# Kernel optimization log

Hardware: AMD Instinct MI355X
Metric: run time of the kernel (lower is better)

## Reference

```python
import jax, jax.numpy as jnp
import numpy as np

N = 50000
E = 800000
NUM_GRAPHS = 64

def gat_layer(x, W, att_src, att_dst, bias, src, dst, heads, out_ch, concat):
    n = x.shape[0]
    h = (x @ W).reshape(n, heads, out_ch)                      # [N,H,C]
    a_s = jnp.sum(h * att_src, axis=-1)                        # [N,H]
    a_d = jnp.sum(h * att_dst, axis=-1)                        # [N,H]
    e = jax.nn.leaky_relu(a_s[src] + a_d[dst], 0.2)            # [E,H]
    m = jax.ops.segment_max(e, dst, num_segments=n)            # segment softmax (self-loops guarantee non-empty)
    e = jnp.exp(e - m[dst])
    s = jax.ops.segment_sum(e, dst, num_segments=n)
    alpha = e / s[dst]                                         # [E,H]
    out = jax.ops.segment_sum(alpha[:, :, None] * h[src], dst, num_segments=n)  # [N,H,C]
    out = out.reshape(n, heads * out_ch) if concat else out.mean(axis=1)
    return out + bias

def setup_inputs() -> dict:
    key = jax.random.key(0)
    ks = jax.random.split(key, 20)
    inp = {}
    inp['x'] = jax.random.normal(ks[0], (N, 256), dtype=jnp.float32)
    inp['edge_index'] = jax.random.randint(ks[1], (2, E), 0, N, dtype=jnp.int64)
    inp['batch'] = jnp.sort(jax.random.randint(ks[2], (N,), 0, NUM_GRAPHS, dtype=jnp.int64))
    s = 0.05
    inp['W1'] = jax.random.normal(ks[3], (256, 256), dtype=jnp.float32) * s
    inp['att_src1'] = jax.random.normal(ks[4], (8, 32), dtype=jnp.float32) * s
    inp['att_dst1'] = jax.random.normal(ks[5], (8, 32), dtype=jnp.float32) * s
    inp['b1'] = jax.random.normal(ks[6], (256,), dtype=jnp.float32) * s
    inp['W2'] = jax.random.normal(ks[7], (256, 256), dtype=jnp.float32) * s
    inp['att_src2'] = jax.random.normal(ks[8], (8, 32), dtype=jnp.float32) * s
    inp['att_dst2'] = jax.random.normal(ks[9], (8, 32), dtype=jnp.float32) * s
    inp['b2'] = jax.random.normal(ks[10], (256,), dtype=jnp.float32) * s
    inp['W3'] = jax.random.normal(ks[11], (256, 32), dtype=jnp.float32) * s
    inp['att_src3'] = jax.random.normal(ks[12], (1, 32), dtype=jnp.float32) * s
    inp['att_dst3'] = jax.random.normal(ks[13], (1, 32), dtype=jnp.float32) * s
    inp['b3'] = jax.random.normal(ks[14], (32,), dtype=jnp.float32) * s
    inp['linW'] = jax.random.normal(ks[15], (32, 1), dtype=jnp.float32) * s
    inp['linb'] = jax.random.normal(ks[16], (1,), dtype=jnp.float32) * s
    return inp

def reference(x, edge_index, batch, W1, att_src1, att_dst1, b1, W2, att_src2, att_dst2, b2,
              W3, att_src3, att_dst3, b3, linW, linb):
    # add self loops (PyG add_self_loops=True)
    loop = jnp.arange(N, dtype=edge_index.dtype)
    src = jnp.concatenate([edge_index[0], loop])
    dst = jnp.concatenate([edge_index[1], loop])
    # eval mode: dropout is identity
    h = gat_layer(x, W1, att_src1, att_dst1, b1, src, dst, 8, 32, True)
    h = jax.nn.elu(h)
    h = gat_layer(h, W2, att_src2, att_dst2, b2, src, dst, 8, 32, True)
    h = jax.nn.elu(h)
    h = gat_layer(h, W3, att_src3, att_dst3, b3, src, dst, 1, 32, False)
    # global mean pool over all nodes (topic_mask defaults to all True)
    sums = jax.ops.segment_sum(h, batch, num_segments=NUM_GRAPHS)
    cnts = jax.ops.segment_sum(jnp.ones((N,), h.dtype), batch, num_segments=NUM_GRAPHS)
    pooled = sums / jnp.maximum(cnts, 1.0)[:, None]
    out = pooled @ linW + linb                                  # [G,1]
    return out.squeeze(-1)                                      # num_classes==2
```

## Files before the change

kernel.cpp:

```cpp
#include <hip/hip_runtime.h>
#include <hip/hip_fp8.h>
#include <math.h>


typedef __attribute__((ext_vector_type(8))) __bf16 bf16x8;
typedef __attribute__((ext_vector_type(4))) __bf16 bf16x4;
typedef __attribute__((ext_vector_type(4))) float f32x4;
typedef __attribute__((ext_vector_type(2))) float f32x2;

#define SCAN_CH 4

__device__ inline unsigned char f32_to_fp8(float f) {
  __hip_fp8_e4m3 v(f);
  return (unsigned char)v.__x;
}
__device__ inline float fp8_to_f32(unsigned char u) {
  __hip_fp8_e4m3 v;
  v.__x = (__hip_fp8_storage_t)u;
  return (float)v;
}

__device__ inline void fma_fp8x4(f32x4& acc, float w, unsigned int packed) {
#if defined(__has_builtin) && __has_builtin(__builtin_amdgcn_cvt_pk_f32_fp8)
  f32x2 lo = __builtin_amdgcn_cvt_pk_f32_fp8((int)packed, false);
  f32x2 hi = __builtin_amdgcn_cvt_pk_f32_fp8((int)packed, true);
  acc[0] += w * lo[0];
  acc[1] += w * lo[1];
  acc[2] += w * hi[0];
  acc[3] += w * hi[1];
#else
  acc[0] += w * fp8_to_f32((unsigned char)(packed & 0xff));
  acc[1] += w * fp8_to_f32((unsigned char)((packed >> 8) & 0xff));
  acc[2] += w * fp8_to_f32((unsigned char)((packed >> 16) & 0xff));
  acc[3] += w * fp8_to_f32((unsigned char)(packed >> 24));
#endif
}

__global__ __launch_bounds__(256) void k_init_deg(int* deg, int N) {
  int n = blockIdx.x * 256 + threadIdx.x;
  if (n < N) deg[n] = 1;
}

__global__ __launch_bounds__(256) void k_count_deg(const int* __restrict__ ei,
                                                   int E, int* deg) {
  int e = blockIdx.x * 256 + threadIdx.x;
  if (e < E) atomicAdd(&deg[ei[E + e]], 1);
}

__global__ __launch_bounds__(256) void k_scan_partial(const int* __restrict__ deg,
                                                      int* __restrict__ blockSums,
                                                      int N) {
  __shared__ int sh[256];
  int t = threadIdx.x, b = blockIdx.x;
  int base = (b * 256 + t) * SCAN_CH;
  int s = 0;
#pragma unroll
  for (int j = 0; j < SCAN_CH; j++) {
    int idx = base + j;
    if (idx < N) s += deg[idx];
  }
  sh[t] = s;
  __syncthreads();
  for (int off = 128; off > 0; off >>= 1) {
    if (t < off) sh[t] += sh[t + off];
    __syncthreads();
  }
  if (t == 0) blockSums[b] = sh[0];
}

__global__ __launch_bounds__(256) void k_scan_blocksums(
    const int* __restrict__ blockSums, int* __restrict__ blockOffs,
    int* __restrict__ rowptr, int nb, int N) {
  __shared__ int sh[256];
  int t = threadIdx.x;
  int v = (t < nb) ? blockSums[t] : 0;
  sh[t] = v;
  __syncthreads();
  for (int off = 1; off < 256; off <<= 1) {
    int u = (t >= off) ? sh[t - off] : 0;
    __syncthreads();
    sh[t] += u;
    __syncthreads();
  }
  if (t < nb) blockOffs[t] = sh[t] - v;
  if (t == nb - 1) rowptr[N] = sh[t];
}

__global__ __launch_bounds__(256) void k_scan_final(const int* __restrict__ deg,
                                                    const int* __restrict__ blockOffs,
                                                    int* __restrict__ rowptr,
                                                    int* __restrict__ cursor, int N) {
  __shared__ int sh[256];
  int t = threadIdx.x, b = blockIdx.x;
  int base = (b * 256 + t) * SCAN_CH;
  int vals[SCAN_CH];
  int s = 0;
#pragma unroll
  for (int j = 0; j < SCAN_CH; j++) {
    int idx = base + j;
    vals[j] = (idx < N) ? deg[idx] : 0;
    s += vals[j];
  }
  sh[t] = s;
  __syncthreads();
  for (int off = 1; off < 256; off <<= 1) {
    int u = (t >= off) ? sh[t - off] : 0;
    __syncthreads();
    sh[t] += u;
    __syncthreads();
  }
  int run = blockOffs[b] + sh[t] - s;
#pragma unroll
  for (int j = 0; j < SCAN_CH; j++) {
    int idx = base + j;
    if (idx < N) {
      rowptr[idx] = run;
      cursor[idx] = run;
      run += vals[j];
    }
  }
}

__global__ __launch_bounds__(256) void k_scatter2(const int* __restrict__ ei,
                                                  int E, int N, int* cursor,
                                                  int2* __restrict__ col2,
                                                  int* __restrict__ col_s,
                                                  int chunkSz) {
  int stripe = blockIdx.x & 7;
  int chunk = blockIdx.x >> 3;
  int lo = (int)(((long long)N * stripe) >> 3);
  int hi = (int)(((long long)N * (stripe + 1)) >> 3);
  int base = chunk * chunkSz;
  int end = base + chunkSz;
  int total = E + N;
  if (end > total) end = total;
  for (int i = base + threadIdx.x; i < end; i += 256) {
    int d = (i < E) ? ei[E + i] : (i - E);
    if (d < lo || d >= hi) continue;
    int s = (i < E) ? ei[i] : d;
    int pos = atomicAdd(&cursor[d], 1);
    col2[pos] = make_int2(s, d);
    col_s[pos] = s;
  }
}

__global__ __launch_bounds__(256) void k_cast(const float* __restrict__ in,
                                              __bf16* __restrict__ oh, int n4) {
  int i = blockIdx.x * 256 + threadIdx.x;
  if (i >= n4) return;
  float4 v = ((const float4*)in)[i];
  bf16x4 h;
  h[0] = (__bf16)v.x;
  h[1] = (__bf16)v.y;
  h[2] = (__bf16)v.z;
  h[3] = (__bf16)v.w;
  ((bf16x4*)oh)[i] = h;
}

__global__ __launch_bounds__(256) void k_wprep(const float* __restrict__ W,
                                               __bf16* __restrict__ WTh,
                                               int K, int Nc) {
  int i = blockIdx.x * 256 + threadIdx.x;
  if (i >= K * Nc) return;
  int n = i / K, k = i - n * K;
  WTh[i] = (__bf16)W[k * Nc + n];
}

__global__ __launch_bounds__(256) void k_gemm_sA(
    const __bf16* __restrict__ Ah, const __bf16* __restrict__ BTh,
    __bf16* __restrict__ Ch, unsigned char* __restrict__ Cf8, int M, int K) {
  constexpr int NcFull = 256;
  __shared__ __bf16 sA[64 * 256];
  int tid = threadIdx.x;
  int lane = tid & 63, wave = tid >> 6;
  int quad = lane >> 4, l16 = lane & 15;
  int m0 = blockIdx.x * 64;
  int col0 = wave * 64;
  int srow = tid >> 2;
  int mtw = srow >> 4, l16w = srow & 15;
  int arow = min(m0 + srow, M - 1);
  const __bf16* ag = Ah + (size_t)arow * K;
#pragma unroll
  for (int r = 0; r < 8; r++) {
    int c = (tid & 3) + r * 4;
    int s = c >> 2, q = c & 3;
    int slot = (((s * 4 + mtw) * 4 + q) * 16 + l16w) * 8;
    *(bf16x8*)(sA + slot) = *(const bf16x8*)(ag + c * 8);
  }
  __syncthreads();
  const __bf16* brh = BTh + (size_t)(col0 + l16) * K + quad * 8;
  f32x4 acc[4][4];
#pragma unroll
  for (int mt = 0; mt < 4; mt++)
#pragma unroll
    for (int t = 0; t < 4; t++) acc[mt][t] = (f32x4){0.f, 0.f, 0.f, 0.f};
  for (int s = 0; s < 8; s++) {
    bf16x8 b_h[4];
#pragma unroll
    for (int t = 0; t < 4; t++)
      b_h[t] = *(const bf16x8*)(brh + (size_t)t * 16 * K + s * 32);
    bf16x8 a_h[4];
#pragma unroll
    for (int mt = 0; mt < 4; mt++)
      a_h[mt] = *(const bf16x8*)(sA + (((s * 4 + mt) * 4 + quad) * 16 + l16) * 8);
#pragma unroll
    for (int t = 0; t < 4; t++) {
#pragma unroll
      for (int mt = 0; mt < 4; mt++) {
        acc[mt][t] = __builtin_amdgcn_mfma_f32_16x16x32_bf16(a_h[mt], b_h[t], acc[mt][t], 0, 0, 0);
      }
    }
  }
#pragma unroll
  for (int mt = 0; mt < 4; mt++) {
#pragma unroll
    for (int t = 0; t < 4; t++) {
#pragma unroll
      for (int r = 0; r < 4; r++) {
        int m = m0 + mt * 16 + quad * 4 + r;
        if (m < M) {
          size_t o = (size_t)m * NcFull + col0 + t * 16 + l16;
          Ch[o] = (__bf16)acc[mt][t][r];
          Cf8[o] = f32_to_fp8(acc[mt][t][r]);
        }
      }
    }
  }
}

template <int NT, int MT>
__global__ __launch_bounds__(256) void k_gemm_split(
    const __bf16* __restrict__ Ah, const __bf16* __restrict__ BTh,
    __bf16* __restrict__ Ch, int M, int K, int NcFull) {
  int lane = threadIdx.x & 63;
  int wave = threadIdx.x >> 6;
  int quad = lane >> 4;
  int l16 = lane & 15;
  int m0 = blockIdx.y * (64 * MT) + wave * (16 * MT);
  int col0 = blockIdx.x * (NT * 16);
  const __bf16* arh[MT];
#pragma unroll
  for (int mt = 0; mt < MT; mt++) {
    int am = min(m0 + mt * 16 + l16, M - 1);
    arh[mt] = Ah + (size_t)am * K + quad * 8;
  }
  const __bf16* brh = BTh + (size_t)(col0 + l16) * K + quad * 8;
  f32x4 acc[MT][NT];
#pragma unroll
  for (int mt = 0; mt < MT; mt++)
#pragma unroll
    for (int t = 0; t < NT; t++) acc[mt][t] = (f32x4){0.f, 0.f, 0.f, 0.f};
  for (int k0 = 0; k0 < K; k0 += 32) {
    bf16x8 a_h[MT], b_h[NT];
#pragma unroll
    for (int mt = 0; mt < MT; mt++) {
      a_h[mt] = *(const bf16x8*)(arh[mt] + k0);
    }
#pragma unroll
    for (int t = 0; t < NT; t++)
      b_h[t] = *(const bf16x8*)(brh + (size_t)t * 16 * K + k0);
#pragma unroll
    for (int t = 0; t < NT; t++) {
#pragma unroll
      for (int mt = 0; mt < MT; mt++) {
        acc[mt][t] = __builtin_amdgcn_mfma_f32_16x16x32_bf16(a_h[mt], b_h[t], acc[mt][t], 0, 0, 0);
      }
    }
  }
#pragma unroll
  for (int mt = 0; mt < MT; mt++) {
#pragma unroll
    for (int t = 0; t < NT; t++) {
#pragma unroll
      for (int r = 0; r < 4; r++) {
        int m = m0 + mt * 16 + quad * 4 + r;
        if (m < M)
          Ch[(size_t)m * NcFull + col0 + t * 16 + l16] = (__bf16)acc[mt][t][r];
      }
    }
  }
}

__global__ __launch_bounds__(256) void k_att(const __bf16* __restrict__ Hh,
                                             const float* __restrict__ attS,
                                             const float* __restrict__ attD,
                                             float* __restrict__ aS,
                                             float* __restrict__ aD, int NH, int H) {
  int idx = blockIdx.x * 256 + threadIdx.x;
  if (idx >= NH) return;
  int h = idx % H;
  const bf16x8* hv = (const bf16x8*)(Hh + (size_t)idx * 32);
  const float* sv = attS + h * 32;
  const float* dv = attD + h * 32;
  float ss = 0.f, dd = 0.f;
#pragma unroll
  for (int k = 0; k < 4; k++) {
    bf16x8 a = hv[k];
#pragma unroll
    for (int j = 0; j < 8; j++) {
      float v = (float)a[j];
      ss += v * sv[k * 8 + j];
      dd += v * dv[k * 8 + j];
    }
  }
  aS[idx] = ss;
  aD[idx] = dd;
}

__global__ __launch_bounds__(256) void k_edge_alpha8(
    const float* __restrict__ aS, const float* __restrict__ aD,
    const int2* __restrict__ col2,
    __bf16* __restrict__ ealpha, int M) {
  int e = blockIdx.x * 256 + threadIdx.x;
  if (e >= M) return;
  int2 sd = col2[e];
  const float* ap = aS + (size_t)sd.x * 8;
  const float* dp = aD + (size_t)sd.y * 8;
  bf16x8 ev;
#pragma unroll
  for (int h = 0; h < 8; h++) {
    float x = ap[h] + dp[h];
    x = (x > 0.f) ? x : 0.2f * x;
    ev[h] = (__bf16)__expf(x);
  }
  *(bf16x8*)(ealpha + (size_t)e * 8) = ev;
}

__global__ __launch_bounds__(256) void k_edge_alpha1(
    const float* __restrict__ aS, const float* __restrict__ aD,
    const int2* __restrict__ col2,
    __bf16* __restrict__ ealpha, int M) {
  int e = blockIdx.x * 256 + threadIdx.x;
  if (e >= M) return;
  int2 sd = col2[e];
  float x = aS[sd.x] + aD[sd.y];
  x = (x > 0.f) ? x : 0.2f * x;
  ealpha[e] = (__bf16)__expf(x);
}

__global__ __launch_bounds__(256) void k_gat_agg8(
    const unsigned char* __restrict__ Hf8, const int* __restrict__ rowptr,
    const int* __restrict__ col_s, const __bf16* __restrict__ ealpha,
    const float* __restrict__ bias, __bf16* __restrict__ outh, int N) {
  int wid = (blockIdx.x * blockDim.x + threadIdx.x) >> 6;
  int lane = threadIdx.x & 63;
  if (wid >= N) return;
  int n = wid;
  int row0 = rowptr[n];
  int deg = rowptr[n + 1] - row0;
  int head = lane >> 3;

  f32x4 acc = (f32x4){0.f, 0.f, 0.f, 0.f};
  float den = 0.f;
  const __bf16* ea = ealpha;
  int i = 0;
  for (; i + 3 < deg; i += 4) {
    int sl = row0 + i;
    int s0 = col_s[sl + 0];
    int s1 = col_s[sl + 1];
    int s2 = col_s[sl + 2];
    int s3 = col_s[sl + 3];
    float w0 = (float)ea[(size_t)(sl + 0) * 8 + head];
    float w1 = (float)ea[(size_t)(sl + 1) * 8 + head];
    float w2 = (float)ea[(size_t)(sl + 2) * 8 + head];
    float w3 = (float)ea[(size_t)(sl + 3) * 8 + head];
    unsigned int p0 = *(const unsigned int*)(Hf8 + (size_t)s0 * 256 + lane * 4);
    unsigned int p1 = *(const unsigned int*)(Hf8 + (size_t)s1 * 256 + lane * 4);
    unsigned int p2 = *(const unsigned int*)(Hf8 + (size_t)s2 * 256 + lane * 4);
    unsigned int p3 = *(const unsigned int*)(Hf8 + (size_t)s3 * 256 + lane * 4);
    den += w0 + w1 + w2 + w3;
    fma_fp8x4(acc, w0, p0);
    fma_fp8x4(acc, w1, p1);
    fma_fp8x4(acc, w2, p2);
    fma_fp8x4(acc, w3, p3);
  }
  for (; i < deg; i++) {
    int sl = row0 + i;
    int s0 = col_s[sl];
    float w0 = (float)ea[(size_t)sl * 8 + head];
    unsigned int p0 = *(const unsigned int*)(Hf8 + (size_t)s0 * 256 + lane * 4);
    den += w0;
    fma_fp8x4(acc, w0, p0);
  }
  float rsv = 1.f / den;
  float4 bv = *(const float4*)(bias + lane * 4);
  bf16x4 hb;
#pragma unroll
  for (int j = 0; j < 4; j++) {
    float v = acc[j] * rsv + ((const float*)&bv)[j];
    v = (v > 0.f) ? v : (__expf(v) - 1.f);
    hb[j] = (__bf16)v;
  }
  *(bf16x4*)(outh + (size_t)n * 256 + lane * 4) = hb;
}

__global__ __launch_bounds__(256) void k_gat_agg1(
    const __bf16* __restrict__ Hh, const int* __restrict__ rowptr,
    const int* __restrict__ col_s, const __bf16* __restrict__ ealpha,
    const float* __restrict__ bias, float* __restrict__ out, int N) {
  int wid = (blockIdx.x * blockDim.x + threadIdx.x) >> 6;
  int lane = threadIdx.x & 63;
  if (wid >= N) return;
  int n = wid;
  int row0 = rowptr[n];
  int deg = rowptr[n + 1] - row0;
  int eo = lane >> 3;
  int cl = lane & 7;
  f32x4 acc = (f32x4){0.f, 0.f, 0.f, 0.f};
  float den = 0.f;
  for (int i = eo; i < deg; i += 8) {
    int slot = row0 + i;
    int src = col_s[slot];
    float w = (float)ealpha[slot];
    den += w;
    bf16x4 hv = *(const bf16x4*)(Hh + (size_t)src * 32 + cl * 4);
#pragma unroll
    for (int j = 0; j < 4; j++) acc[j] += w * (float)hv[j];
  }
#pragma unroll
  for (int off = 8; off < 64; off <<= 1) {
#pragma unroll
    for (int j = 0; j < 4; j++) acc[j] += __shfl_xor(acc[j], off, 64);
    den += __shfl_xor(den, off, 64);
  }
  if (eo == 0) {
    float rsv = 1.f / den;
#pragma unroll
    for (int j = 0; j < 4; j++)
      out[(size_t)n * 32 + cl * 4 + j] = acc[j] * rsv + bias[cl * 4 + j];
  }
}

__global__ __launch_bounds__(256) void k_pool_final(
    const float* __restrict__ h, const int* __restrict__ batch,
    const float* __restrict__ linW, const float* __restrict__ linb,
    float* __restrict__ out, int N) {
  __shared__ float sh[256];
  int g = blockIdx.x;
  int tid = threadIdx.x;
  int grp = tid >> 5, c = tid & 31;
  int lo = 0, hi = N;
  while (lo < hi) { int mid = (lo + hi) >> 1; if (batch[mid] < g) lo = mid + 1; else hi = mid; }
  int start = lo;
  hi = N;
  while (lo < hi) { int mid = (lo + hi) >> 1; if (batch[mid] < g + 1) lo = mid + 1; else hi = mid; }
  int end = lo;
  float acc = 0.f;
  for (int n = start + grp; n < end; n += 8) acc += h[(size_t)n * 32 + c];
  sh[tid] = acc;
  __syncthreads();
  if (tid < 32) {
    float s = 0.f;
#pragma unroll
    for (int j = 0; j < 8; j++) s += sh[j * 32 + tid];
    float v = s * linW[tid];
#pragma unroll
    for (int off = 16; off > 0; off >>= 1) v += __shfl_xor(v, off, 64);
    if (tid == 0) {
      float cnt = (float)(end - start);
      out[g] = v / fmaxf(cnt, 1.f) + linb[0];
    }
  }
}

extern "C" void kernel_launch(void* const* d_in, const int* in_sizes, int n_in,
                              void* d_out, int out_size, void* d_ws, size_t ws_size,
                              hipStream_t stream) {
  const float* x = (const float*)d_in[0];
  const int* ei = (const int*)d_in[1];
  const int* batch = (const int*)d_in[2];
  const float* W1 = (const float*)d_in[3];
  const float* as1 = (const float*)d_in[4];
  const float* ad1 = (const float*)d_in[5];
  const float* b1 = (const float*)d_in[6];
  const float* W2 = (const float*)d_in[7];
  const float* as2 = (const float*)d_in[8];
  const float* ad2 = (const float*)d_in[9];
  const float* b2 = (const float*)d_in[10];
  const float* W3 = (const float*)d_in[11];
  const float* as3 = (const float*)d_in[12];
  const float* ad3 = (const float*)d_in[13];
  const float* b3 = (const float*)d_in[14];
  const float* linW = (const float*)d_in[15];
  const float* linb = (const float*)d_in[16];

  const int N = in_sizes[0] / 256;
  const int E = in_sizes[1] / 2;
  const int NUM_GRAPHS = 64;
  float* out = (float*)d_out;

  char* ws = (char*)d_ws;
  size_t off = 0;
  auto alloc = [&](size_t bytes) -> void* {
    void* p = ws + off;
    off += (bytes + 255) & ~(size_t)255;
    return p;
  };
  __bf16* Hh = (__bf16*)alloc((size_t)N * 256 * 2);
  unsigned char* Hf8 = (unsigned char*)alloc((size_t)N * 256);
  __bf16* Ah = (__bf16*)alloc((size_t)N * 256 * 2);
  __bf16* ealpha = (__bf16*)alloc((size_t)(E + N) * 8 * 2);
  float* aS = (float*)alloc((size_t)N * 8 * 4);
  float* aD = (float*)alloc((size_t)N * 8 * 4);
  int* deg = (int*)alloc((size_t)N * 4);
  int* rowptr = (int*)alloc((size_t)(N + 1) * 4);
  int* cursor = (int*)alloc((size_t)(N + 1) * 4);
  int2* col2 = (int2*)alloc((size_t)(E + N) * 8);
  int* col_s = (int*)alloc((size_t)(E + N) * 4);
  int* blockSums = (int*)alloc(256 * 4);
  int* blockOffs = (int*)alloc(256 * 4);
  __bf16* WT1h = (__bf16*)alloc(256 * 256 * 2);
  __bf16* WT2h = (__bf16*)alloc(256 * 256 * 2);
  __bf16* WT3h = (__bf16*)alloc(32 * 256 * 2);
  float* h3agg = (float*)Ah;

  k_cast<<<(N * 64 + 255) / 256, 256, 0, stream>>>(x, Ah, N * 64);
  k_wprep<<<(256 * 256 + 255) / 256, 256, 0, stream>>>(W1, WT1h, 256, 256);
  k_wprep<<<(256 * 256 + 255) / 256, 256, 0, stream>>>(W2, WT2h, 256, 256);
  k_wprep<<<(256 * 32 + 255) / 256, 256, 0, stream>>>(W3, WT3h, 256, 32);
  k_init_deg<<<(N + 255) / 256, 256, 0, stream>>>(deg, N);
  k_count_deg<<<(E + 255) / 256, 256, 0, stream>>>(ei, E, deg);
  const int nb = (N + 256 * SCAN_CH - 1) / (256 * SCAN_CH);
  k_scan_partial<<<nb, 256, 0, stream>>>(deg, blockSums, N);
  k_scan_blocksums<<<1, 256, 0, stream>>>(blockSums, blockOffs, rowptr, nb, N);
  k_scan_final<<<nb, 256, 0, stream>>>(deg, blockOffs, rowptr, cursor, N);
  {
    const int totalItems = E + N;
    const int nch = 256;
    const int chunkSz = (totalItems + nch - 1) / nch;
    k_scatter2<<<8 * nch, 256, 0, stream>>>(ei, E, N, cursor, col2, col_s, chunkSz);
  }

  const int aggBlocks = (N + 3) / 4;
  const int gemmBlocks = (N + 63) / 64;
  const int M = E + N;
  const int edgeBlocks = (M + 255) / 256;
  dim3 g3(1, (N + 63) / 64);

  k_gemm_sA<<<gemmBlocks, 256, 0, stream>>>(Ah, WT1h, Hh, Hf8, N, 256);
  k_att<<<(N * 8 + 255) / 256, 256, 0, stream>>>(Hh, as1, ad1, aS, aD, N * 8, 8);
  k_edge_alpha8<<<edgeBlocks, 256, 0, stream>>>(aS, aD, col2, ealpha, M);
  k_gat_agg8<<<aggBlocks, 256, 0, stream>>>(Hf8, rowptr, col_s, ealpha, b1,
                                            Ah, N);
  k_gemm_sA<<<gemmBlocks, 256, 0, stream>>>(Ah, WT2h, Hh, Hf8, N, 256);
  k_att<<<(N * 8 + 255) / 256, 256, 0, stream>>>(Hh, as2, ad2, aS, aD, N * 8, 8);
  k_edge_alpha8<<<edgeBlocks, 256, 0, stream>>>(aS, aD, col2, ealpha, M);
  k_gat_agg8<<<aggBlocks, 256, 0, stream>>>(Hf8, rowptr, col_s, ealpha, b2,
                                            Ah, N);
  k_gemm_split<2, 1><<<g3, 256, 0, stream>>>(Ah, WT3h, Hh, N, 256, 32);
  k_att<<<(N + 255) / 256, 256, 0, stream>>>(Hh, as3, ad3, aS, aD, N, 1);
  k_edge_alpha1<<<edgeBlocks, 256, 0, stream>>>(aS, aD, col2, ealpha, M);
  k_gat_agg1<<<aggBlocks, 256, 0, stream>>>(Hh, rowptr, col_s, ealpha, b3,
                                            h3agg, N);
  k_pool_final<<<NUM_GRAPHS, 256, 0, stream>>>(h3agg, batch, linW, linb, out, N);
}
```

Baseline: 483.0 us.

## Fuse edge attention weights into aggregation and drop col_s array

Removes the separate edge-alpha kernels and computes each edge's leaky-relu and exp inside the aggregation kernels from aS and aD. This avoids writing and re-reading the per-edge bf16 alpha buffer and saves three launches. The 8-head aggregation is restructured so each wave handles 4 edges at a time, with 16 lanes each loading 16 fp8 bytes and a shuffle reduction at the end. The col_s array is dropped and sources are read from col2. The trade-off is exp work repeated per lane, strided int2 reads, and extra shuffle reductions.

```diff
diff --git a/kernel.cpp b/kernel.cpp
--- a/kernel.cpp
+++ b/kernel.cpp
@@ -124,7 +124,6 @@
 __global__ __launch_bounds__(256) void k_scatter2(const int* __restrict__ ei,
                                                   int E, int N, int* cursor,
                                                   int2* __restrict__ col2,
-                                                  int* __restrict__ col_s,
                                                   int chunkSz) {
   int stripe = blockIdx.x & 7;
   int chunk = blockIdx.x >> 3;
@@ -140,7 +139,6 @@
     int s = (i < E) ? ei[i] : d;
     int pos = atomicAdd(&cursor[d], 1);
     col2[pos] = make_int2(s, d);
-    col_s[pos] = s;
   }
 }
 
@@ -307,97 +305,98 @@
   aD[idx] = dd;
 }
 
-__global__ __launch_bounds__(256) void k_edge_alpha8(
-    const float* __restrict__ aS, const float* __restrict__ aD,
-    const int2* __restrict__ col2,
-    __bf16* __restrict__ ealpha, int M) {
-  int e = blockIdx.x * 256 + threadIdx.x;
-  if (e >= M) return;
-  int2 sd = col2[e];
-  const float* ap = aS + (size_t)sd.x * 8;
-  const float* dp = aD + (size_t)sd.y * 8;
-  bf16x8 ev;
-#pragma unroll
-  for (int h = 0; h < 8; h++) {
-    float x = ap[h] + dp[h];
-    x = (x > 0.f) ? x : 0.2f * x;
-    ev[h] = (__bf16)__expf(x);
-  }
-  *(bf16x8*)(ealpha + (size_t)e * 8) = ev;
-}
-
-__global__ __launch_bounds__(256) void k_edge_alpha1(
-    const float* __restrict__ aS, const float* __restrict__ aD,
-    const int2* __restrict__ col2,
-    __bf16* __restrict__ ealpha, int M) {
-  int e = blockIdx.x * 256 + threadIdx.x;
-  if (e >= M) return;
-  int2 sd = col2[e];
-  float x = aS[sd.x] + aD[sd.y];
-  x = (x > 0.f) ? x : 0.2f * x;
-  ealpha[e] = (__bf16)__expf(x);
-}
-
-__global__ __launch_bounds__(256) void k_gat_agg8(
+__global__ __launch_bounds__(256) void k_gat_agg8f(
     const unsigned char* __restrict__ Hf8, const int* __restrict__ rowptr,
-    const int* __restrict__ col_s, const __bf16* __restrict__ ealpha,
-    const float* __restrict__ bias, __bf16* __restrict__ outh, int N) {
+    const int2* __restrict__ col2, const float* __restrict__ aS,
+    const float* __restrict__ aD, const float* __restrict__ bias,
+    __bf16* __restrict__ outh, int N) {
   int wid = (blockIdx.x * blockDim.x + threadIdx.x) >> 6;
   int lane = threadIdx.x & 63;
   if (wid >= N) return;
   int n = wid;
   int row0 = rowptr[n];
   int deg = rowptr[n + 1] - row0;
-  int head = lane >> 3;
-
-  f32x4 acc = (f32x4){0.f, 0.f, 0.f, 0.f};
+  int g = lane >> 4;
+  int c = lane & 15;
+  int head = c >> 1;
+  float ad = aD[(size_t)n * 8 + head];
+  f32x4 acc0 = (f32x4){0.f, 0.f, 0.f, 0.f};
+  f32x4 acc1 = (f32x4){0.f, 0.f, 0.f, 0.f};
+  f32x4 acc2 = (f32x4){0.f, 0.f, 0.f, 0.f};
+  f32x4 acc3 = (f32x4){0.f, 0.f, 0.f, 0.f};
   float den = 0.f;
-  const __bf16* ea = ealpha;
-  int i = 0;
-  for (; i + 3 < deg; i += 4) {
-    int sl = row0 + i;
-    int s0 = col_s[sl + 0];
-    int s1 = col_s[sl + 1];
-    int s2 = col_s[sl + 2];
-    int s3 = col_s[sl + 3];
-    float w0 = (float)ea[(size_t)(sl + 0) * 8 + head];
-    float w1 = (float)ea[(size_t)(sl + 1) * 8 + head];
-    float w2 = (float)ea[(size_t)(sl + 2) * 8 + head];
-    float w3 = (float)ea[(size_t)(sl + 3) * 8 + head];
-    unsigned int p0 = *(const unsigned int*)(Hf8 + (size_t)s0 * 256 + lane * 4);
-    unsigned int p1 = *(const unsigned int*)(Hf8 + (size_t)s1 * 256 + lane * 4);
-    unsigned int p2 = *(const unsigned int*)(Hf8 + (size_t)s2 * 256 + lane * 4);
-    unsigned int p3 = *(const unsigned int*)(Hf8 + (size_t)s3 * 256 + lane * 4);
-    den += w0 + w1 + w2 + w3;
-    fma_fp8x4(acc, w0, p0);
-    fma_fp8x4(acc, w1, p1);
-    fma_fp8x4(acc, w2, p2);
-    fma_fp8x4(acc, w3, p3);
-  }
-  for (; i < deg; i++) {
-    int sl = row0 + i;
-    int s0 = col_s[sl];
-    float w0 = (float)ea[(size_t)sl * 8 + head];
-    unsigned int p0 = *(const unsigned int*)(Hf8 + (size_t)s0 * 256 + lane * 4);
-    den += w0;
-    fma_fp8x4(acc, w0, p0);
-  }
-  float rsv = 1.f / den;
-  float4 bv = *(const float4*)(bias + lane * 4);
-  bf16x4 hb;
-#pragma unroll
-  for (int j = 0; j < 4; j++) {
-    float v = acc[j] * rsv + ((const float*)&bv)[j];
-    v = (v > 0.f) ? v : (__expf(v) - 1.f);
-    hb[j] = (__bf16)v;
-  }
-  *(bf16x4*)(outh + (size_t)n * 256 + lane * 4) = hb;
-}
-
-__global__ __launch_bounds__(256) void k_gat_agg1(
+  int dm1 = deg - 1;
+  const int* colx = (const int*)col2;
+  for (int i = 0; i < deg; i += 8) {
+    int e0 = i + g, e1 = i + 4 + g;
+    int sl0 = row0 + min(e0, dm1);
+    int sl1 = row0 + min(e1, dm1);
+    int s0 = colx[(size_t)sl0 * 2];
+    int s1 = colx[(size_t)sl1 * 2];
+    uint4 p0 = *(const uint4*)(Hf8 + (size_t)s0 * 256 + c * 16);
+    uint4 p1 = *(const uint4*)(Hf8 + (size_t)s1 * 256 + c * 16);
+    float w0 = 0.f, w1 = 0.f;
+    if (e0 < deg) {
+      float x = aS[(size_t)s0 * 8 + head] + ad;
+      x = (x > 0.f) ? x : 0.2f * x;
+      w0 = __expf(x);
+    }
+    if (e1 < deg) {
+      float x = aS[(size_t)s1 * 8 + head] + ad;
+      x = (x > 0.f) ? x : 0.2f * x;
+      w1 = __expf(x);
+    }
+    den += w0 + w1;
+    fma_fp8x4(acc0, w0, p0.x);
+    fma_fp8x4(acc1, w0, p0.y);
+    fma_fp8x4(acc2, w0, p0.z);
+    fma_fp8x4(acc3, w0, p0.w);
+    fma_fp8x4(acc0, w1, p1.x);
+    fma_fp8x4(acc1, w1, p1.y);
+    fma_fp8x4(acc2, w1, p1.z);
+    fma_fp8x4(acc3, w1, p1.w);
+  }
+#pragma unroll
+  for (int off = 16; off < 64; off <<= 1) {
+#pragma unroll
+    for (int j = 0; j < 4; j++) {
+      acc0[j] += __shfl_xor(acc0[j], off, 64);
+      acc1[j] += __shfl_xor(acc1[j], off, 64);
+      acc2[j] += __shfl_xor(acc2[j], off, 64);
+      acc3[j] += __shfl_xor(acc3[j], off, 64);
+    }
+    den += __shfl_xor(den, off, 64);
+  }
+  if (g == 0) {
+    float rsv = 1.f / den;
+    const float4* bp = (const float4*)(bias + c * 16);
+    float4 b0 = bp[0], b1 = bp[1], b2 = bp[2], b3 = bp[3];
+    bf16x8 o0, o1;
+#pragma unroll
+    for (int j = 0; j < 4; j++) {
+      float v0 = acc0[j] * rsv + ((const float*)&b0)[j];
+      float v1 = acc1[j] * rsv + ((const float*)&b1)[j];
+      float v2 = acc2[j] * rsv + ((const float*)&b2)[j];
+      float v3 = acc3[j] * rsv + ((const float*)&b3)[j];
+      v0 = (v0 > 0.f) ? v0 : (__expf(v0) - 1.f);
+      v1 = (v1 > 0.f) ? v1 : (__expf(v1) - 1.f);
+      v2 = (v2 > 0.f) ? v2 : (__expf(v2) - 1.f);
+      v3 = (v3 > 0.f) ? v3 : (__expf(v3) - 1.f);
+      o0[j] = (__bf16)v0;
+      o0[j + 4] = (__bf16)v1;
+      o1[j] = (__bf16)v2;
+      o1[j + 4] = (__bf16)v3;
+    }
+    *(bf16x8*)(outh + (size_t)n * 256 + c * 16) = o0;
+    *(bf16x8*)(outh + (size_t)n * 256 + c * 16 + 8) = o1;
+  }
+}
+
+__global__ __launch_bounds__(256) void k_gat_agg1f(
     const __bf16* __restrict__ Hh, const int* __restrict__ rowptr,
-    const int* __restrict__ col_s, const __bf16* __restrict__ ealpha,
-    const float* __restrict__ bias, float* __restrict__ out, int N) {
+    const int2* __restrict__ col2, const float* __restrict__ aS,
+    const float* __restrict__ aD, const float* __restrict__ bias,
+    float* __restrict__ out, int N) {
   int wid = (blockIdx.x * blockDim.x + threadIdx.x) >> 6;
   int lane = threadIdx.x & 63;
   if (wid >= N) return;
@@ -406,12 +405,16 @@
   int deg = rowptr[n + 1] - row0;
   int eo = lane >> 3;
   int cl = lane & 7;
+  float ad = aD[n];
+  const int* colx = (const int*)col2;
   f32x4 acc = (f32x4){0.f, 0.f, 0.f, 0.f};
   float den = 0.f;
   for (int i = eo; i < deg; i += 8) {
     int slot = row0 + i;
-    int src = col_s[slot];
-    float w = (float)ealpha[slot];
+    int src = colx[(size_t)slot * 2];
+    float x = aS[src] + ad;
+    x = (x > 0.f) ? x : 0.2f * x;
+    float w = __expf(x);
     den += w;
     bf16x4 hv = *(const bf16x4*)(Hh + (size_t)src * 32 + cl * 4);
 #pragma unroll
@@ -499,14 +502,12 @@
   __bf16* Hh = (__bf16*)alloc((size_t)N * 256 * 2);
   unsigned char* Hf8 = (unsigned char*)alloc((size_t)N * 256);
   __bf16* Ah = (__bf16*)alloc((size_t)N * 256 * 2);
-  __bf16* ealpha = (__bf16*)alloc((size_t)(E + N) * 8 * 2);
   float* aS = (float*)alloc((size_t)N * 8 * 4);
   float* aD = (float*)alloc((size_t)N * 8 * 4);
   int* deg = (int*)alloc((size_t)N * 4);
   int* rowptr = (int*)alloc((size_t)(N + 1) * 4);
   int* cursor = (int*)alloc((size_t)(N + 1) * 4);
   int2* col2 = (int2*)alloc((size_t)(E + N) * 8);
-  int* col_s = (int*)alloc((size_t)(E + N) * 4);
   int* blockSums = (int*)alloc(256 * 4);
   int* blockOffs = (int*)alloc(256 * 4);
   __bf16* WT1h = (__bf16*)alloc(256 * 256 * 2);
@@ -528,29 +529,24 @@
     const int totalItems = E + N;
     const int nch = 256;
     const int chunkSz = (totalItems + nch - 1) / nch;
-    k_scatter2<<<8 * nch, 256, 0, stream>>>(ei, E, N, cursor, col2, col_s, chunkSz);
+    k_scatter2<<<8 * nch, 256, 0, stream>>>(ei, E, N, cursor, col2, chunkSz);
   }
 
   const int aggBlocks = (N + 3) / 4;
   const int gemmBlocks = (N + 63) / 64;
-  const int M = E + N;
-  const int edgeBlocks = (M + 255) / 256;
   dim3 g3(1, (N + 63) / 64);
 
   k_gemm_sA<<<gemmBlocks, 256, 0, stream>>>(Ah, WT1h, Hh, Hf8, N, 256);
   k_att<<<(N * 8 + 255) / 256, 256, 0, stream>>>(Hh, as1, ad1, aS, aD, N * 8, 8);
-  k_edge_alpha8<<<edgeBlocks, 256, 0, stream>>>(aS, aD, col2, ealpha, M);
-  k_gat_agg8<<<aggBlocks, 256, 0, stream>>>(Hf8, rowptr, col_s, ealpha, b1,
-                                            Ah, N);
+  k_gat_agg8f<<<aggBlocks, 256, 0, stream>>>(Hf8, rowptr, col2, aS, aD, b1,
+                                             Ah, N);
   k_gemm_sA<<<gemmBlocks, 256, 0, stream>>>(Ah, WT2h, Hh, Hf8, N, 256);
   k_att<<<(N * 8 + 255) / 256, 256, 0, stream>>>(Hh, as2, ad2, aS, aD, N * 8, 8);
-  k_edge_alpha8<<<edgeBlocks, 256, 0, stream>>>(aS, aD, col2, ealpha, M);
-  k_gat_agg8<<<aggBlocks, 256, 0, stream>>>(Hf8, rowptr, col_s, ealpha, b2,
-                                            Ah, N);
+  k_gat_agg8f<<<aggBlocks, 256, 0, stream>>>(Hf8, rowptr, col2, aS, aD, b2,
+                                             Ah, N);
   k_gemm_split<2, 1><<<g3, 256, 0, stream>>>(Ah, WT3h, Hh, N, 256, 32);
   k_att<<<(N + 255) / 256, 256, 0, stream>>>(Hh, as3, ad3, aS, aD, N, 1);
-  k_edge_alpha1<<<edgeBlocks, 256, 0, stream>>>(aS, aD, col2, ealpha, M);
-  k_gat_agg1<<<aggBlocks, 256, 0, stream>>>(Hh, rowptr, col_s, ealpha, b3,
-                                            h3agg, N);
+  k_gat_agg1f<<<aggBlocks, 256, 0, stream>>>(Hh, rowptr, col2, aS, aD, b3,
+                                             h3agg, N);
   k_pool_final<<<NUM_GRAPHS, 256, 0, stream>>>(h3agg, batch, linW, linb, out, N);
 }
```

New measurement: 463.0 us. -4.1%, faster.
